# Kernel optimization log

Measured on AMD Instinct MI355X. Metric: run time of the kernel, lower is better.

The kernel has to match this reference:

```python
import jax, jax.numpy as jnp
import numpy as np

MAX_LEN = 1024

def _make_pe():
    # matches TemporalPositionalEncoding buffer construction
    pe = np.zeros(MAX_LEN, np.float32)
    pos = np.arange(MAX_LEN, dtype=np.float64)
    d = MAX_LEN + 1e-9
    pe[0::2] = np.sin(pos[0::2] / 10000.0 ** (pos[0::2] / d))
    pe[1::2] = np.cos(pos[1::2] / 10000.0 ** (pos[1::2] / d))
    return jnp.asarray(pe, jnp.float32)


def setup_inputs() -> dict:
    key = jax.random.key(0)
    k1, k2, k3, k4, k5 = jax.random.split(key, 5)
    B, H, W, C = 16, 56, 56, 768
    sw = 4
    x = jax.random.normal(k1, (B, H, W, C), dtype=jnp.float32)
    # source inits these to zero; use small random weights so the op is non-trivial
    qkv_w = jax.random.normal(k2, (3 * sw, sw), dtype=jnp.float32) * 0.1
    qkv_b = jax.random.normal(k3, (3 * sw,), dtype=jnp.float32) * 0.1
    proj_w = jax.random.normal(k4, (C, C), dtype=jnp.float32) * 0.02
    proj_b = jax.random.normal(k5, (C,), dtype=jnp.float32) * 0.02
    pe = _make_pe()
    return {"x": x, "qkv_w": qkv_w, "qkv_b": qkv_b,
            "proj_w": proj_w, "proj_b": proj_b, "pe": pe}


def reference(x, qkv_w, qkv_b, proj_w, proj_b, pe):
    B, H, W, C = x.shape
    sw = qkv_w.shape[0] // 3  # group_size
    # temporal positional encoding along channel dim
    x = x + pe[:C].astype(x.dtype).reshape(1, 1, 1, -1)
    pad = (-C) % sw  # static Python int
    if pad:
        x = jnp.pad(x, ((0, 0), (0, 0), (0, 0), (0, pad)))
    Cp = x.shape[-1]
    N = Cp // sw
    xg = x.reshape(B * H * W, N, sw)  # [G, N, sw]
    qkv = xg @ qkv_w.T + qkv_b        # [G, N, 3*sw]
    q, k, v = jnp.split(qkv, 3, axis=-1)
    # SDPA with q,k,v of shape [G, N, 1, sw]: seq length (L=S=1) attention.
    # softmax over the single key is identically 1, so out == v; we keep the
    # explicit score/softmax for structural fidelity (it's scalar-per-group).
    scale = 1.0 / jnp.sqrt(jnp.asarray(sw, x.dtype))
    scores = jnp.einsum('gnd,gnd->gn', q, k) * scale          # [G, N]
    attn = jax.nn.softmax(scores[..., None, None], axis=-1)   # [G, N, 1, 1] == 1
    out = attn[..., 0] * v                                    # [G, N, sw]
    out = out.reshape(B, H, W, Cp)[..., :C]
    return out @ proj_w.T + proj_b
```

## Files before the change

### kernel.cpp

```cpp
#include <hip/hip_runtime.h>
#include <hip/hip_bf16.h>

typedef __attribute__((ext_vector_type(8))) short bf16x8;
typedef __attribute__((ext_vector_type(4))) float f32x4;
typedef __attribute__((ext_vector_type(4))) unsigned short u16x4;
typedef unsigned short u16;

#define M_DIM 50176
#define N_DIM 768
#define K_DIM 768

__device__ __forceinline__ u16 f2bf(float f) {
    __hip_bfloat16 h = __float2bfloat16(f);
    return *reinterpret_cast<u16*>(&h);
}

__device__ __forceinline__ void gld_lds16(const void* g, void* l) {
    __builtin_amdgcn_global_load_lds(
        (const __attribute__((address_space(1))) unsigned int*)g,
        (__attribute__((address_space(3))) unsigned int*)l, 16, 0, 0);
}

__global__ void fold_weights(const float* __restrict__ qkv_w,
                             const float* __restrict__ qkv_b,
                             const float* __restrict__ proj_w,
                             const float* __restrict__ proj_b,
                             const float* __restrict__ pe,
                             u16* __restrict__ Bw, float* __restrict__ bias) {
    const int o = blockIdx.x;
    const int t = threadIdx.x;
    __shared__ float wv[16];
    __shared__ float bv4[4];
    __shared__ float red[4];
    if (t < 16) wv[t] = qkv_w[32 + t];
    if (t < 4)  bv4[t] = qkv_b[8 + t];
    __syncthreads();
    const float* Prow = proj_w + o * 768;
    float s = 0.f;
    for (int c = t; c < 768; c += 256) {
        int g4 = c & ~3, j = c & 3;
        float af = Prow[g4 + 0] * wv[0 * 4 + j] + Prow[g4 + 1] * wv[1 * 4 + j] +
                   Prow[g4 + 2] * wv[2 * 4 + j] + Prow[g4 + 3] * wv[3 * 4 + j];
        Bw[o * 768 + c] = f2bf(af);
        s += af * pe[c];
        s += Prow[c] * bv4[j];
    }
    #pragma unroll
    for (int off = 32; off; off >>= 1) s += __shfl_down(s, off, 64);
    if ((t & 63) == 0) red[t >> 6] = s;
    __syncthreads();
    if (t == 0) bias[o] = red[0] + red[1] + red[2] + red[3] + proj_b[o];
}

__global__ __launch_bounds__(256, 3)
void gemm_fused(const float* __restrict__ X, const u16* __restrict__ Bw,
                const float* __restrict__ bias, float* __restrict__ Y) {
    const int b = blockIdx.x;
    const int bid = (b & 7) * 294 + (b >> 3);
    const int mt = bid / 6, nt = bid - mt * 6;
    const int m0 = mt * 128, n0 = nt * 128;

    const int tid = threadIdx.x;
    const int lane = tid & 63;
    const int w = tid >> 6;
    const int wm = w >> 1, wn = w & 1;

    __shared__ u16 As[128 * 64];
    __shared__ u16 Bs[2][128 * 64];

    f32x4 acc[4][4];
    #pragma unroll
    for (int i = 0; i < 4; ++i)
        #pragma unroll
        for (int j = 0; j < 4; ++j)
            acc[i][j] = (f32x4){0.f, 0.f, 0.f, 0.f};

    const int arow = tid >> 4;
    const int agg  = tid & 15;
    const int bg = lane & 7;

    float4 R[8];

    auto load_a = [&](int k0) {
        const float4* src = (const float4*)(X + (long)m0 * K_DIM + k0);
        #pragma unroll
        for (int i = 0; i < 8; ++i) {
            int r = arow + 16 * i;
            R[i] = src[(long)r * (K_DIM / 4) + agg];
        }
    };

    auto write_a = [&]() {
        #pragma unroll
        for (int i = 0; i < 8; ++i) {
            int r = arow + 16 * i;
            int pb = (agg * 8) ^ ((r & 7) << 4);
            u16x4 hv;
            hv.x = f2bf(R[i].x);
            hv.y = f2bf(R[i].y);
            hv.z = f2bf(R[i].z);
            hv.w = f2bf(R[i].w);
            *(u16x4*)&As[r * 64 + (pb >> 1)] = hv;
        }
    };

    auto stage_b = [&](int buf, int k0) {
        #pragma unroll
        for (int j = 0; j < 4; ++j) {
            int rowbase = j * 32 + w * 8;
            int row = rowbase + (lane >> 3);
            const char* src = (const char*)Bw + ((long)(n0 + row) * K_DIM + k0) * 2 +
                              ((bg * 16) ^ ((row & 7) << 4));
            gld_lds16(src, (void*)&Bs[buf][rowbase * 64]);
        }
    };

    auto compute = [&](int bb) {
        #pragma unroll
        for (int h = 0; h < 2; ++h) {
            bf16x8 av[4], bv_[4];
            #pragma unroll
            for (int mf = 0; mf < 4; ++mf) {
                int r = wm * 64 + mf * 16 + (lane & 15);
                int pb = (h * 64 + ((lane >> 4) << 4)) ^ ((r & 7) << 4);
                av[mf] = *(const bf16x8*)&As[r * 64 + (pb >> 1)];
            }
            #pragma unroll
            for (int nf = 0; nf < 4; ++nf) {
                int r = wn * 64 + nf * 16 + (lane & 15);
                int pb = (h * 64 + ((lane >> 4) << 4)) ^ ((r & 7) << 4);
                bv_[nf] = *(const bf16x8*)&Bs[bb][r * 64 + (pb >> 1)];
            }
            __builtin_amdgcn_s_setprio(1);
            #pragma unroll
            for (int mf = 0; mf < 4; ++mf)
                #pragma unroll
                for (int nf = 0; nf < 4; ++nf)
                    acc[mf][nf] = __builtin_amdgcn_mfma_f32_16x16x32_bf16(
                        av[mf], bv_[nf], acc[mf][nf], 0, 0, 0);
            __builtin_amdgcn_s_setprio(0);
        }
    };

    stage_b(0, 0);
    load_a(0);
    write_a();
    __syncthreads();

    const int NT = K_DIM / 64;
    #pragma unroll 1
    for (int t = 0; t < NT - 1; ++t) {
        stage_b((t + 1) & 1, (t + 1) * 64);
        load_a((t + 1) * 64);
        compute(t & 1);
        __syncthreads();
        write_a();
        __syncthreads();
    }
    compute((NT - 1) & 1);

    const int colq = lane & 15;
    const int rowq = (lane >> 4) * 4;
    #pragma unroll
    for (int nf = 0; nf < 4; ++nf) {
        int col = n0 + wn * 64 + nf * 16 + colq;
        float bi = bias[col];
        #pragma unroll
        for (int mf = 0; mf < 4; ++mf) {
            long rbase = m0 + wm * 64 + mf * 16 + rowq;
            #pragma unroll
            for (int r = 0; r < 4; ++r) {
                __builtin_nontemporal_store(acc[mf][nf][r] + bi,
                                            &Y[(rbase + r) * N_DIM + col]);
            }
        }
    }
}

extern "C" void kernel_launch(void* const* d_in, const int* in_sizes, int n_in,
                              void* d_out, int out_size, void* d_ws, size_t ws_size,
                              hipStream_t stream) {
    const float* x      = (const float*)d_in[0];
    const float* qkv_w  = (const float*)d_in[1];
    const float* qkv_b  = (const float*)d_in[2];
    const float* proj_w = (const float*)d_in[3];
    const float* proj_b = (const float*)d_in[4];
    const float* pe     = (const float*)d_in[5];
    float* y = (float*)d_out;

    u16*   Bw   = (u16*)d_ws;
    float* bias = (float*)((char*)d_ws + (size_t)N_DIM * K_DIM * 2);

    fold_weights<<<768, 256, 0, stream>>>(qkv_w, qkv_b, proj_w, proj_b, pe, Bw, bias);
    gemm_fused<<<(M_DIM / 128) * (N_DIM / 128), 256, 0, stream>>>(x, Bw, bias, y);
}
```

Before: 113.8 us.

## Load A fragments directly into registers, dropping the LDS staging for A

Each wave now owns 32 full rows of the 128x128 tile and reads its A fragments straight from global memory into MFMA operand registers, converting fp32 to bf16 in registers. The shared-memory A buffer and one barrier per k-step go away. In exchange, B fragment reads from LDS double (every wave reads all 128 columns), and the per-lane global A loads are less coalesced (32-byte pieces spread across rows).

Result: slower. 271.6 us (+138.6%).

```diff
diff --git a/kernel.cpp b/kernel.cpp
--- a/kernel.cpp
+++ b/kernel.cpp
@@ -3,7 +3,6 @@
 
 typedef __attribute__((ext_vector_type(8))) short bf16x8;
 typedef __attribute__((ext_vector_type(4))) float f32x4;
-typedef __attribute__((ext_vector_type(4))) unsigned short u16x4;
 typedef unsigned short u16;
 
 #define M_DIM 50176
@@ -63,44 +62,49 @@
     const int tid = threadIdx.x;
     const int lane = tid & 63;
     const int w = tid >> 6;
-    const int wm = w >> 1, wn = w & 1;
 
-    __shared__ u16 As[128 * 64];
     __shared__ u16 Bs[2][128 * 64];
 
-    f32x4 acc[4][4];
+    f32x4 acc[2][8];
     #pragma unroll
-    for (int i = 0; i < 4; ++i)
+    for (int i = 0; i < 2; ++i)
         #pragma unroll
-        for (int j = 0; j < 4; ++j)
+        for (int j = 0; j < 8; ++j)
             acc[i][j] = (f32x4){0.f, 0.f, 0.f, 0.f};
 
-    const int arow = tid >> 4;
-    const int agg  = tid & 15;
     const int bg = lane & 7;
+
+    const int arow = m0 + w * 32 + (lane & 15);
+    const int akoff = (lane >> 4) * 8;
 
     float4 R[8];
 
     auto load_a = [&](int k0) {
-        const float4* src = (const float4*)(X + (long)m0 * K_DIM + k0);
         #pragma unroll
-        for (int i = 0; i < 8; ++i) {
-            int r = arow + 16 * i;
-            R[i] = src[(long)r * (K_DIM / 4) + agg];
-        }
+        for (int mf = 0; mf < 2; ++mf)
+            #pragma unroll
+            for (int h = 0; h < 2; ++h) {
+                const float4* src = (const float4*)(X + (long)(arow + mf * 16) * K_DIM +
+                                                    k0 + h * 32 + akoff);
+                R[(mf * 2 + h) * 2 + 0] = src[0];
+                R[(mf * 2 + h) * 2 + 1] = src[1];
+            }
     };
 
-    auto write_a = [&]() {
+    bf16x8 av[4];
+    auto cvt_a = [&]() {
         #pragma unroll
-        for (int i = 0; i < 8; ++i) {
-            int r = arow + 16 * i;
-            int pb = (agg * 8) ^ ((r & 7) << 4);
-            u16x4 hv;
-            hv.x = f2bf(R[i].x);
-            hv.y = f2bf(R[i].y);
-            hv.z = f2bf(R[i].z);
-            hv.w = f2bf(R[i].w);
-            *(u16x4*)&As[r * 64 + (pb >> 1)] = hv;
+        for (int f = 0; f < 4; ++f) {
+            bf16x8 v;
+            v[0] = (short)f2bf(R[f * 2 + 0].x);
+            v[1] = (short)f2bf(R[f * 2 + 0].y);
+            v[2] = (short)f2bf(R[f * 2 + 0].z);
+            v[3] = (short)f2bf(R[f * 2 + 0].w);
+            v[4] = (short)f2bf(R[f * 2 + 1].x);
+            v[5] = (short)f2bf(R[f * 2 + 1].y);
+            v[6] = (short)f2bf(R[f * 2 + 1].z);
+            v[7] = (short)f2bf(R[f * 2 + 1].w);
+            av[f] = v;
         }
     };
 
@@ -118,56 +122,49 @@
     auto compute = [&](int bb) {
         #pragma unroll
         for (int h = 0; h < 2; ++h) {
-            bf16x8 av[4], bv_[4];
+            bf16x8 bv_[8];
             #pragma unroll
-            for (int mf = 0; mf < 4; ++mf) {
-                int r = wm * 64 + mf * 16 + (lane & 15);
-                int pb = (h * 64 + ((lane >> 4) << 4)) ^ ((r & 7) << 4);
-                av[mf] = *(const bf16x8*)&As[r * 64 + (pb >> 1)];
-            }
-            #pragma unroll
-            for (int nf = 0; nf < 4; ++nf) {
-                int r = wn * 64 + nf * 16 + (lane & 15);
+            for (int nf = 0; nf < 8; ++nf) {
+                int r = nf * 16 + (lane & 15);
                 int pb = (h * 64 + ((lane >> 4) << 4)) ^ ((r & 7) << 4);
                 bv_[nf] = *(const bf16x8*)&Bs[bb][r * 64 + (pb >> 1)];
             }
             __builtin_amdgcn_s_setprio(1);
             #pragma unroll
-            for (int mf = 0; mf < 4; ++mf)
+            for (int mf = 0; mf < 2; ++mf)
                 #pragma unroll
-                for (int nf = 0; nf < 4; ++nf)
+                for (int nf = 0; nf < 8; ++nf)
                     acc[mf][nf] = __builtin_amdgcn_mfma_f32_16x16x32_bf16(
-                        av[mf], bv_[nf], acc[mf][nf], 0, 0, 0);
+                        av[mf * 2 + h], bv_[nf], acc[mf][nf], 0, 0, 0);
             __builtin_amdgcn_s_setprio(0);
         }
     };
 
     stage_b(0, 0);
     load_a(0);
-    write_a();
     __syncthreads();
 
     const int NT = K_DIM / 64;
     #pragma unroll 1
     for (int t = 0; t < NT - 1; ++t) {
+        cvt_a();
         stage_b((t + 1) & 1, (t + 1) * 64);
         load_a((t + 1) * 64);
         compute(t & 1);
         __syncthreads();
-        write_a();
-        __syncthreads();
     }
+    cvt_a();
     compute((NT - 1) & 1);
 
     const int colq = lane & 15;
     const int rowq = (lane >> 4) * 4;
     #pragma unroll
-    for (int nf = 0; nf < 4; ++nf) {
-        int col = n0 + wn * 64 + nf * 16 + colq;
+    for (int nf = 0; nf < 8; ++nf) {
+        int col = n0 + nf * 16 + colq;
         float bi = bias[col];
         #pragma unroll
-        for (int mf = 0; mf < 4; ++mf) {
-            long rbase = m0 + wm * 64 + mf * 16 + rowq;
+        for (int mf = 0; mf < 2; ++mf) {
+            long rbase = m0 + w * 32 + mf * 16 + rowq;
             #pragma unroll
             for (int r = 0; r < 4; ++r) {
                 __builtin_nontemporal_store(acc[mf][nf][r] + bi,
```

## Load B fragments directly from global and double-buffer A in LDS

Applied to the files above, without the earlier changes.

Stops staging the folded weight matrix through shared memory. Each wave now loads its B fragments straight from global memory into registers, relying on L2/L1 caching of the small weight matrix. The freed LDS space double-buffers the A tile, so the bf16 conversion and store of the next tile overlaps the current compute, with one barrier per k-step instead of two. The risk is that direct global B loads inside the MFMA loop expose latency and add cache traffic.

Result: slower. 185.3 us (+62.8%).

```diff
diff --git a/kernel.cpp b/kernel.cpp
--- a/kernel.cpp
+++ b/kernel.cpp
@@ -13,12 +13,6 @@
 __device__ __forceinline__ u16 f2bf(float f) {
     __hip_bfloat16 h = __float2bfloat16(f);
     return *reinterpret_cast<u16*>(&h);
-}
-
-__device__ __forceinline__ void gld_lds16(const void* g, void* l) {
-    __builtin_amdgcn_global_load_lds(
-        (const __attribute__((address_space(1))) unsigned int*)g,
-        (__attribute__((address_space(3))) unsigned int*)l, 16, 0, 0);
 }
 
 __global__ void fold_weights(const float* __restrict__ qkv_w,
@@ -65,8 +59,7 @@
     const int w = tid >> 6;
     const int wm = w >> 1, wn = w & 1;
 
-    __shared__ u16 As[128 * 64];
-    __shared__ u16 Bs[2][128 * 64];
+    __shared__ u16 As[2][128 * 64];
 
     f32x4 acc[4][4];
     #pragma unroll
@@ -77,7 +70,6 @@
 
     const int arow = tid >> 4;
     const int agg  = tid & 15;
-    const int bg = lane & 7;
 
     float4 R[8];
 
@@ -90,7 +82,7 @@
         }
     };
 
-    auto write_a = [&]() {
+    auto write_a = [&](int buf) {
         #pragma unroll
         for (int i = 0; i < 8; ++i) {
             int r = arow + 16 * i;
@@ -100,36 +92,24 @@
             hv.y = f2bf(R[i].y);
             hv.z = f2bf(R[i].z);
             hv.w = f2bf(R[i].w);
-            *(u16x4*)&As[r * 64 + (pb >> 1)] = hv;
+            *(u16x4*)&As[buf][r * 64 + (pb >> 1)] = hv;
         }
     };
 
-    auto stage_b = [&](int buf, int k0) {
-        #pragma unroll
-        for (int j = 0; j < 4; ++j) {
-            int rowbase = j * 32 + w * 8;
-            int row = rowbase + (lane >> 3);
-            const char* src = (const char*)Bw + ((long)(n0 + row) * K_DIM + k0) * 2 +
-                              ((bg * 16) ^ ((row & 7) << 4));
-            gld_lds16(src, (void*)&Bs[buf][rowbase * 64]);
-        }
-    };
+    const u16* bbase = Bw + (long)(n0 + wn * 64 + (lane & 15)) * K_DIM + (lane >> 4) * 8;
 
-    auto compute = [&](int bb) {
+    auto compute = [&](int ab, int k0) {
         #pragma unroll
         for (int h = 0; h < 2; ++h) {
             bf16x8 av[4], bv_[4];
             #pragma unroll
+            for (int nf = 0; nf < 4; ++nf)
+                bv_[nf] = *(const bf16x8*)(bbase + (long)nf * 16 * K_DIM + k0 + h * 32);
+            #pragma unroll
             for (int mf = 0; mf < 4; ++mf) {
                 int r = wm * 64 + mf * 16 + (lane & 15);
                 int pb = (h * 64 + ((lane >> 4) << 4)) ^ ((r & 7) << 4);
-                av[mf] = *(const bf16x8*)&As[r * 64 + (pb >> 1)];
-            }
-            #pragma unroll
-            for (int nf = 0; nf < 4; ++nf) {
-                int r = wn * 64 + nf * 16 + (lane & 15);
-                int pb = (h * 64 + ((lane >> 4) << 4)) ^ ((r & 7) << 4);
-                bv_[nf] = *(const bf16x8*)&Bs[bb][r * 64 + (pb >> 1)];
+                av[mf] = *(const bf16x8*)&As[ab][r * 64 + (pb >> 1)];
             }
             __builtin_amdgcn_s_setprio(1);
             #pragma unroll
@@ -142,22 +122,26 @@
         }
     };
 
-    stage_b(0, 0);
     load_a(0);
-    write_a();
+    write_a(0);
+    load_a(64);
     __syncthreads();
 
-    const int NT = K_DIM / 64;
     #pragma unroll 1
-    for (int t = 0; t < NT - 1; ++t) {
-        stage_b((t + 1) & 1, (t + 1) * 64);
-        load_a((t + 1) * 64);
-        compute(t & 1);
+    for (int t2 = 0; t2 < 10; t2 += 2) {
+        write_a(1);
+        load_a((t2 + 2) * 64);
+        compute(0, t2 * 64);
         __syncthreads();
-        write_a();
+        write_a(0);
+        load_a((t2 + 3) * 64);
+        compute(1, (t2 + 1) * 64);
         __syncthreads();
     }
-    compute((NT - 1) & 1);
+    write_a(1);
+    compute(0, 10 * 64);
+    __syncthreads();
+    compute(1, 11 * 64);
 
     const int colq = lane & 15;
     const int rowq = (lane >> 4) * 4;
```
